# Performance work log

Measured on AMD Instinct MI355X. Metric: run time of the kernel, lower is better.

Reference implementation:

```python
import jax, jax.numpy as jnp
import numpy as np

# Static module config (matches init_kwargs; note forward requires P == Np)
Np = 60   # particles
P  = 60   # per-particle features
Nv = 14   # secondary vertices
S  = 5    # per-vertex features
De = 20
Do = 24
HID = 60
NPP = Np * (Np - 1)
NPV = Np * Nv

# Edge list replacing the dense one-hot Rr/Rs matmuls.
# Edges are all ordered pairs (i, j), i != j, ordered by receiver i then sender j,
# so edges with the same receiver are contiguous (enables reshape+sum scatter).
_pairs = np.array([(i, j) for i in range(Np) for j in range(Np) if i != j], dtype=np.int64)
RECV = jnp.asarray(_pairs[:, 0])  # [NPP]
SEND = jnp.asarray(_pairs[:, 1])  # [NPP]


def _mlp(h, W1, b1, W2, b2):
    return jax.nn.relu(h @ W1 + b1) @ W2 + b2


def setup_inputs() -> dict:
    key = jax.random.key(0)
    ks = jax.random.split(key, 9)
    B = 1024

    def lin(k, fi, fo):
        kw, kb = jax.random.split(k)
        s = 1.0 / np.sqrt(fi)
        W = jax.random.uniform(kw, (fi, fo), minval=-s, maxval=s, dtype=jnp.float32)
        b = jax.random.uniform(kb, (fo,), minval=-s, maxval=s, dtype=jnp.float32)
        return W, b

    W1_pp, b1_pp = lin(ks[0], 2 * P, HID)
    W2_pp, b2_pp = lin(ks[1], HID, De)
    W1_pv, b1_pv = lin(ks[2], P + S, HID)
    W2_pv, b2_pv = lin(ks[3], HID, De)
    W1_o, b1_o = lin(ks[4], P + De, HID)
    W2_o, b2_o = lin(ks[5], HID, Do)
    Wc, bc = lin(ks[6], Do, 1)
    x = jax.random.normal(ks[7], (B, P, Np), dtype=jnp.float32)
    y = jax.random.normal(ks[8], (B, S, Nv), dtype=jnp.float32)
    return dict(x=x, y=y,
                W1_pp=W1_pp, b1_pp=b1_pp, W2_pp=W2_pp, b2_pp=b2_pp,
                W1_pv=W1_pv, b1_pv=b1_pv, W2_pv=W2_pv, b2_pv=b2_pv,
                W1_o=W1_o, b1_o=b1_o, W2_o=W2_o, b2_o=b2_o,
                Wc=Wc, bc=bc)


def reference(x, y, W1_pp, b1_pp, W2_pp, b2_pp, W1_pv, b1_pv, W2_pv, b2_pv,
              W1_o, b1_o, W2_o, b2_o, Wc, bc):
    Bb = x.shape[0]
    # particle-particle branch: gather (x @ Rr, x @ Rs) as index takes
    Orr = jnp.take(x, RECV, axis=2)                  # [B, P, NPP]
    Ors = jnp.take(x, SEND, axis=2)                  # [B, P, NPP]
    Bcat = jnp.concatenate([Orr, Ors], axis=1)       # [B, 2P, NPP]
    # Faithful to the original: B.view(-1, 2P) WITHOUT transposing (row-major flatten)
    E = _mlp(Bcat.reshape(-1, 2 * P), W1_pp, b1_pp, W2_pp, b2_pp).reshape(Bb, NPP, De)
    E = jnp.swapaxes(E, 1, 2)                        # [B, De, NPP]
    # scatter-sum E @ Rr.T : edges grouped by receiver -> reshape+sum
    Ebar_pp = E.reshape(Bb, De, Np, Np - 1).sum(axis=-1)   # [B, De, Np]
    # particle-vertex branch: t = i*Nv + v
    Ork = jnp.repeat(x, Nv, axis=2)                  # [B, P, NPV]  (x @ Rk)
    Orv = jnp.tile(y, (1, 1, Np))                    # [B, S, NPV]  (y @ Rv)
    C = jnp.swapaxes(jnp.concatenate([Ork, Orv], axis=1), 1, 2)  # [B, NPV, P+S]
    F = _mlp(C.reshape(-1, P + S), W1_pv, b1_pv, W2_pv, b2_pv).reshape(Bb, NPV, De)
    F = jnp.swapaxes(F, 1, 2)                        # [B, De, NPV]
    Ebar_pv = F.reshape(Bb, De, Np, Nv).sum(axis=-1)  # F @ Rk.T  -> [B, De, Np]
    Ebar = jnp.swapaxes(Ebar_pp + Ebar_pv, 1, 2)     # [B, Np, De]
    J = jnp.concatenate([x, Ebar], axis=2)           # [B, Np, P+De] (requires P==Np)
    O = _mlp(J.reshape(-1, P + De), W1_o, b1_o, W2_o, b2_o).reshape(Bb, Np, Do)
    O = O.sum(axis=1)                                # transpose+sum over particles -> [B, Do]
    O = O @ Wc + bc                                  # [B, 1]
    return jax.nn.sigmoid(O)
```

## Files before the change

kernel.cpp:

```cpp
#include <hip/hip_runtime.h>
#include <hip/hip_bf16.h>
#include <math.h>

typedef __attribute__((ext_vector_type(8))) short short8;
typedef __attribute__((ext_vector_type(4))) float f32x4;

namespace {
constexpr int XP = 61;
constexpr int EB0 = 3660;
constexpr int Y0 = 4860;
constexpr int ZSLOT = 4930;
constexpr int ARENA_W = 4931;

constexpr int NTAB_PP = 222 * 4 * 64 * 8;
constexpr int NTAB_PV = 53 * 3 * 64 * 8;
constexpr int NTAB_O  = 4 * 3 * 64 * 8;
constexpr int TABPP_B = 0;
constexpr int TABPV_B = 909312;
constexpr int TABO_B  = 1072128;
constexpr int WPP1_B  = 1084416;
constexpr int WPP2_B  = 1100800;
constexpr int WPV1_B  = 1104896;
constexpr int WPV2_B  = 1117184;
constexpr int WO1_B   = 1121280;
constexpr int WO2_B   = 1133568;
constexpr int BIAS_B  = 1137664;
}

__device__ __forceinline__ short f2bfs(float f) {
  __hip_bfloat16 h = __float2bfloat16(f);
  short s;
  __builtin_memcpy(&s, &h, 2);
  return s;
}

__global__ __launch_bounds__(256) void build_tables(char* wsb) {
  int t = blockIdx.x * 256 + threadIdx.x;
  unsigned short* tpp = (unsigned short*)(wsb + TABPP_B);
  unsigned short* tpv = (unsigned short*)(wsb + TABPV_B);
  unsigned short* tou = (unsigned short*)(wsb + TABO_B);
  if (t < NTAB_PP) {
    int j = t & 7, l = (t >> 3) & 63, blk = t >> 9;
    int ks = blk & 3, mt = blk >> 2;
    int rr = mt * 16 + (l & 15), k = ks * 32 + (l >> 4) * 8 + j;
    unsigned off = ZSLOT;
    if (rr < 3540 && k < 120) {
      unsigned p = (unsigned)rr * 120u + (unsigned)k;
      unsigned f = p / 3540u, e = p - f * 3540u;
      unsigned i = e / 59u, jj = e - i * 59u;
      unsigned col = (f < 60u) ? i : ((jj < i) ? jj : jj + 1u);
      unsigned ft = (f < 60u) ? f : f - 60u;
      off = ft * (unsigned)XP + col;
    }
    tpp[t] = (unsigned short)off;
    return;
  }
  t -= NTAB_PP;
  if (t < NTAB_PV) {
    int j = t & 7, l = (t >> 3) & 63, blk = t >> 9;
    int ks = blk % 3, mt = blk / 3;
    int tt = mt * 16 + (l & 15), k = ks * 32 + (l >> 4) * 8 + j;
    unsigned off = ZSLOT;
    if (tt < 840 && k < 65) {
      int i = tt / 14, v = tt - i * 14;
      off = (k < 60) ? (unsigned)(k * XP + i) : (unsigned)(Y0 + (k - 60) * 14 + v);
    }
    tpv[t] = (unsigned short)off;
    return;
  }
  t -= NTAB_PV;
  if (t < NTAB_O) {
    int j = t & 7, l = (t >> 3) & 63, blk = t >> 9;
    int ks = blk % 3, mt = blk / 3;
    int r = mt * 16 + (l & 15), k = ks * 32 + (l >> 4) * 8 + j;
    unsigned off = ZSLOT;
    if (r < 60 && k < 80)
      off = (k < 60) ? (unsigned)(r * XP + k) : (unsigned)(EB0 + r * 20 + (k - 60));
    tou[t] = (unsigned short)off;
  }
}

__global__ __launch_bounds__(256) void build_wfrag(char* wsb,
    const float* W1pp, const float* W2pp, const float* W1pv, const float* W2pv,
    const float* W1o, const float* W2o,
    const float* b1pp, const float* b2pp, const float* b1pv, const float* b2pv,
    const float* b1o, const float* b2o) {
  int t = blockIdx.x * 256 + threadIdx.x;
  if (t < 13312) {
    const float* W; int Kt, Nt, NTt; unsigned* dst; int local;
    if (t < 4096)       { W = W1pp; Kt = 120; Nt = 60; NTt = 4; dst = (unsigned*)(wsb + WPP1_B); local = t; }
    else if (t < 5120)  { W = W2pp; Kt = 60;  Nt = 20; NTt = 2; dst = (unsigned*)(wsb + WPP2_B); local = t - 4096; }
    else if (t < 8192)  { W = W1pv; Kt = 65;  Nt = 60; NTt = 4; dst = (unsigned*)(wsb + WPV1_B); local = t - 5120; }
    else if (t < 9216)  { W = W2pv; Kt = 60;  Nt = 20; NTt = 2; dst = (unsigned*)(wsb + WPV2_B); local = t - 8192; }
    else if (t < 12288) { W = W1o;  Kt = 80;  Nt = 60; NTt = 4; dst = (unsigned*)(wsb + WO1_B);  local = t - 9216; }
    else                { W = W2o;  Kt = 60;  Nt = 24; NTt = 2; dst = (unsigned*)(wsb + WO2_B);  local = t - 12288; }
    int d = local & 3, l = (local >> 2) & 63, rest = local >> 8;
    int nt = rest % NTt, ks = rest / NTt;
    int k = ks * 32 + (l >> 4) * 8 + 2 * d, n = nt * 16 + (l & 15);
    float v0 = (k < Kt && n < Nt) ? W[k * Nt + n] : 0.f;
    float v1 = (k + 1 < Kt && n < Nt) ? W[(k + 1) * Nt + n] : 0.f;
    unsigned u0 = (unsigned short)f2bfs(v0);
    unsigned u1 = (unsigned short)f2bfs(v1);
    dst[local] = u0 | (u1 << 16);
    return;
  }
  t -= 13312;
  if (t < 288) {
    float* bd = (float*)(wsb + BIAS_B);
    float v = 0.f;
    if (t < 64)       { if (t < 60) v = b1pp[t]; }
    else if (t < 96)  { int n = t - 64;  if (n < 20) v = b2pp[n]; }
    else if (t < 160) { int n = t - 96;  if (n < 60) v = b1pv[n]; }
    else if (t < 192) { int n = t - 160; if (n < 20) v = b2pv[n]; }
    else if (t < 256) { int n = t - 192; if (n < 60) v = b1o[n]; }
    else              { int n = t - 256; if (n < 24) v = b2o[n]; }
    bd[t] = v;
  }
}

template <int NKS>
__device__ __forceinline__ void mlp_tile(
    int mt, int lane, const uint4* __restrict__ tab,
    const short8 (&bf1)[NKS * 4], const short8 (&bf2)[4],
    const float* __restrict__ biasf, int b1off, int b2off,
    const float* arena, short (*hrow)[72], f32x4 (&a2)[2]) {
  const int cl = lane & 15, qq = lane >> 4;
  f32x4 acc[4];
#pragma unroll
  for (int nt = 0; nt < 4; ++nt) {
    float bv = biasf[b1off + nt * 16 + cl];
    acc[nt] = (f32x4){bv, bv, bv, bv};
  }
#pragma unroll
  for (int ks = 0; ks < NKS; ++ks) {
    uint4 tw = tab[(mt * NKS + ks) * 64 + lane];
    float g0 = arena[tw.x & 0xffffu];
    float g1 = arena[tw.x >> 16];
    float g2 = arena[tw.y & 0xffffu];
    float g3 = arena[tw.y >> 16];
    float g4 = arena[tw.z & 0xffffu];
    float g5 = arena[tw.z >> 16];
    float g6 = arena[tw.w & 0xffffu];
    float g7 = arena[tw.w >> 16];
    short8 af;
    af[0] = f2bfs(g0); af[1] = f2bfs(g1); af[2] = f2bfs(g2); af[3] = f2bfs(g3);
    af[4] = f2bfs(g4); af[5] = f2bfs(g5); af[6] = f2bfs(g6); af[7] = f2bfs(g7);
#pragma unroll
    for (int nt = 0; nt < 4; ++nt)
      acc[nt] = __builtin_amdgcn_mfma_f32_16x16x32_bf16(af, bf1[ks * 4 + nt], acc[nt], 0, 0, 0);
  }
#pragma unroll
  for (int nt = 0; nt < 4; ++nt)
#pragma unroll
    for (int r = 0; r < 4; ++r)
      hrow[qq * 4 + r][nt * 16 + cl] = f2bfs(fmaxf(acc[nt][r], 0.f));
#pragma unroll
  for (int nt = 0; nt < 2; ++nt) {
    float bv = biasf[b2off + nt * 16 + cl];
    a2[nt] = (f32x4){bv, bv, bv, bv};
  }
#pragma unroll
  for (int k2 = 0; k2 < 2; ++k2) {
    short8 af2 = *(const short8*)&hrow[cl][k2 * 32 + qq * 8];
#pragma unroll
    for (int nt = 0; nt < 2; ++nt)
      a2[nt] = __builtin_amdgcn_mfma_f32_16x16x32_bf16(af2, bf2[k2 * 2 + nt], a2[nt], 0, 0, 0);
  }
}

__global__ __launch_bounds__(256, 2) void fused_kernel(
    const float* __restrict__ x, const float* __restrict__ y,
    const float* __restrict__ Wc, const float* __restrict__ Bc,
    const char* __restrict__ wsb, float* __restrict__ out) {
  __shared__ float arena[ARENA_W];
  __shared__ short hlds[4][16][72];
  __shared__ float osum[24];

  const int b = blockIdx.x;
  const int tid = threadIdx.x;
  const int w = tid >> 6;
  const int lane = tid & 63;
  const int cl = lane & 15, qq = lane >> 4, q4 = (lane >> 4) * 4;

  for (int k = tid; k < 3600; k += 256) {
    int r = k / 60, c = k - r * 60;
    arena[r * XP + c] = x[(size_t)b * 3600 + k];
  }
  if (tid < 70) arena[Y0 + tid] = y[(size_t)b * 70 + tid];
  for (int k = tid; k < 1200; k += 256) arena[EB0 + k] = 0.f;
  if (tid == 0) arena[ZSLOT] = 0.f;
  if (tid < 24) osum[tid] = 0.f;
  __syncthreads();

  const float* biasf = (const float*)(wsb + BIAS_B);

  {
    const short8* wf1 = (const short8*)(wsb + WPP1_B);
    const short8* wf2 = (const short8*)(wsb + WPP2_B);
    short8 bf1[16], bf2[4];
#pragma unroll
    for (int i = 0; i < 16; ++i) bf1[i] = wf1[i * 64 + lane];
#pragma unroll
    for (int i = 0; i < 4; ++i) bf2[i] = wf2[i * 64 + lane];
    const uint4* tab = (const uint4*)(wsb + TABPP_B);

    for (int mt = w; mt < 222; mt += 4) {
      f32x4 a2[2];
      mlp_tile<4>(mt, lane, tab, bf1, bf2, biasf, 0, 64, arena, hlds[w], a2);
      int rb = mt * 16 + q4;
      int riA = rb / 59, riB = (rb + 3) / 59;
#pragma unroll
      for (int nt = 0; nt < 2; ++nt) {
        int col = nt * 16 + cl;
        if (col < 20) {
          if (riA == riB && rb + 3 < 3540) {
            atomicAdd(&arena[EB0 + riA * 20 + col],
                      a2[nt][0] + a2[nt][1] + a2[nt][2] + a2[nt][3]);
          } else {
#pragma unroll
            for (int r = 0; r < 4; ++r) {
              int rr = rb + r;
              if (rr < 3540) atomicAdd(&arena[EB0 + (rr / 59) * 20 + col], a2[nt][r]);
            }
          }
        }
      }
    }
  }

  {
    const short8* wf1 = (const short8*)(wsb + WPV1_B);
    const short8* wf2 = (const short8*)(wsb + WPV2_B);
    short8 bf1[12], bf2[4];
#pragma unroll
    for (int i = 0; i < 12; ++i) bf1[i] = wf1[i * 64 + lane];
#pragma unroll
    for (int i = 0; i < 4; ++i) bf2[i] = wf2[i * 64 + lane];
    const uint4* tab = (const uint4*)(wsb + TABPV_B);

    for (int mt = w; mt < 53; mt += 4) {
      f32x4 a2[2];
      mlp_tile<3>(mt, lane, tab, bf1, bf2, biasf, 96, 160, arena, hlds[w], a2);
      int rb = mt * 16 + q4;
      int riA = rb / 14, riB = (rb + 3) / 14;
#pragma unroll
      for (int nt = 0; nt < 2; ++nt) {
        int col = nt * 16 + cl;
        if (col < 20) {
          if (riA == riB && rb + 3 < 840) {
            atomicAdd(&arena[EB0 + riA * 20 + col],
                      a2[nt][0] + a2[nt][1] + a2[nt][2] + a2[nt][3]);
          } else {
#pragma unroll
            for (int r = 0; r < 4; ++r) {
              int tt = rb + r;
              if (tt < 840) atomicAdd(&arena[EB0 + (tt / 14) * 20 + col], a2[nt][r]);
            }
          }
        }
      }
    }
  }

  __syncthreads();

  {
    const short8* wf1 = (const short8*)(wsb + WO1_B);
    const short8* wf2 = (const short8*)(wsb + WO2_B);
    short8 bf1[12], bf2[4];
#pragma unroll
    for (int i = 0; i < 12; ++i) bf1[i] = wf1[i * 64 + lane];
#pragma unroll
    for (int i = 0; i < 4; ++i) bf2[i] = wf2[i * 64 + lane];
    const uint4* tab = (const uint4*)(wsb + TABO_B);

    f32x4 a2[2];
    mlp_tile<3>(w, lane, tab, bf1, bf2, biasf, 192, 256, arena, hlds[w], a2);
    int rb = w * 16 + q4;
#pragma unroll
    for (int nt = 0; nt < 2; ++nt) {
      int col = nt * 16 + cl;
      if (col < 24) {
        if (rb + 3 < 60) {
          atomicAdd(&osum[col], a2[nt][0] + a2[nt][1] + a2[nt][2] + a2[nt][3]);
        } else {
#pragma unroll
          for (int r = 0; r < 4; ++r) {
            if (rb + r < 60) atomicAdd(&osum[col], a2[nt][r]);
          }
        }
      }
    }
  }

  __syncthreads();
  if (tid == 0) {
    float sd = Bc[0];
#pragma unroll
    for (int o = 0; o < 24; ++o) sd = fmaf(osum[o], Wc[o], sd);
    out[b] = 1.f / (1.f + expf(-sd));
  }
}

extern "C" void kernel_launch(void* const* d_in, const int* in_sizes, int n_in,
                              void* d_out, int out_size, void* d_ws, size_t ws_size,
                              hipStream_t stream) {
  const float* x     = (const float*)d_in[0];
  const float* y     = (const float*)d_in[1];
  const float* W1_pp = (const float*)d_in[2];
  const float* b1_pp = (const float*)d_in[3];
  const float* W2_pp = (const float*)d_in[4];
  const float* b2_pp = (const float*)d_in[5];
  const float* W1_pv = (const float*)d_in[6];
  const float* b1_pv = (const float*)d_in[7];
  const float* W2_pv = (const float*)d_in[8];
  const float* b2_pv = (const float*)d_in[9];
  const float* W1_o  = (const float*)d_in[10];
  const float* b1_o  = (const float*)d_in[11];
  const float* W2_o  = (const float*)d_in[12];
  const float* b2_o  = (const float*)d_in[13];
  const float* Wc    = (const float*)d_in[14];
  const float* bc    = (const float*)d_in[15];
  float* out = (float*)d_out;
  char* wsb = (char*)d_ws;

  const int Bb = in_sizes[0] / 3600;
  const int tab_total = NTAB_PP + NTAB_PV + NTAB_O;

  build_tables<<<(tab_total + 255) / 256, 256, 0, stream>>>(wsb);
  build_wfrag<<<(13600 + 255) / 256, 256, 0, stream>>>(wsb,
      W1_pp, W2_pp, W1_pv, W2_pv, W1_o, W2_o,
      b1_pp, b2_pp, b1_pv, b2_pv, b1_o, b2_o);
  fused_kernel<<<Bb, 256, 0, stream>>>(x, y, Wc, bc, wsb, out);
}
```

Baseline: 347.4 us.

## Process two MLP tiles per wave, stream weights from memory, raise occupancy

Weight fragments are no longer held in registers. They are now read from global memory on every k-step, which frees VGPRs and allows the launch bound to go from 2 to 4 blocks per CU. Each wave now processes two row tiles at a time, so one weight load feeds two MFMAs and the LDS gathers of the two tiles can interleave. The gather tables now store byte offsets to drop an address shift, and bias values are hoisted into registers. The cost is more global/L1 weight traffic per MFMA and double the LDS hidden buffer per wave, which could limit the occupancy gain.

```diff
diff --git a/kernel.cpp b/kernel.cpp
--- a/kernel.cpp
+++ b/kernel.cpp
@@ -16,15 +16,15 @@
 constexpr int NTAB_PV = 53 * 3 * 64 * 8;
 constexpr int NTAB_O  = 4 * 3 * 64 * 8;
 constexpr int TABPP_B = 0;
-constexpr int TABPV_B = 909312;
-constexpr int TABO_B  = 1072128;
-constexpr int WPP1_B  = 1084416;
-constexpr int WPP2_B  = 1100800;
-constexpr int WPV1_B  = 1104896;
-constexpr int WPV2_B  = 1117184;
-constexpr int WO1_B   = 1121280;
-constexpr int WO2_B   = 1133568;
-constexpr int BIAS_B  = 1137664;
+constexpr int TABPV_B = TABPP_B + NTAB_PP * 2;
+constexpr int TABO_B  = TABPV_B + NTAB_PV * 2;
+constexpr int WPP1_B  = TABO_B + NTAB_O * 2;
+constexpr int WPP2_B  = WPP1_B + 16 * 64 * 16;
+constexpr int WPV1_B  = WPP2_B + 4 * 64 * 16;
+constexpr int WPV2_B  = WPV1_B + 12 * 64 * 16;
+constexpr int WO1_B   = WPV2_B + 4 * 64 * 16;
+constexpr int WO2_B   = WO1_B + 12 * 64 * 16;
+constexpr int BIAS_B  = WO2_B + 4 * 64 * 16;
 }
 
 __device__ __forceinline__ short f2bfs(float f) {
@@ -52,7 +52,7 @@
       unsigned ft = (f < 60u) ? f : f - 60u;
       off = ft * (unsigned)XP + col;
     }
-    tpp[t] = (unsigned short)off;
+    tpp[t] = (unsigned short)(off * 4u);
     return;
   }
   t -= NTAB_PP;
@@ -65,7 +65,7 @@
       int i = tt / 14, v = tt - i * 14;
       off = (k < 60) ? (unsigned)(k * XP + i) : (unsigned)(Y0 + (k - 60) * 14 + v);
     }
-    tpv[t] = (unsigned short)off;
+    tpv[t] = (unsigned short)(off * 4u);
     return;
   }
   t -= NTAB_PV;
@@ -76,7 +76,7 @@
     unsigned off = ZSLOT;
     if (r < 60 && k < 80)
       off = (k < 60) ? (unsigned)(r * XP + k) : (unsigned)(EB0 + r * 20 + (k - 60));
-    tou[t] = (unsigned short)off;
+    tou[t] = (unsigned short)(off * 4u);
   }
 }
 
@@ -118,69 +118,121 @@
   }
 }
 
-template <int NKS>
-__device__ __forceinline__ void mlp_tile(
-    int mt, int lane, const uint4* __restrict__ tab,
-    const short8 (&bf1)[NKS * 4], const short8 (&bf2)[4],
-    const float* __restrict__ biasf, int b1off, int b2off,
-    const float* arena, short (*hrow)[72], f32x4 (&a2)[2]) {
+__device__ __forceinline__ short8 gather8(const char* xb, uint4 tw) {
+  float g0 = *(const float*)(xb + (tw.x & 0xffffu));
+  float g1 = *(const float*)(xb + (tw.x >> 16));
+  float g2 = *(const float*)(xb + (tw.y & 0xffffu));
+  float g3 = *(const float*)(xb + (tw.y >> 16));
+  float g4 = *(const float*)(xb + (tw.z & 0xffffu));
+  float g5 = *(const float*)(xb + (tw.z >> 16));
+  float g6 = *(const float*)(xb + (tw.w & 0xffffu));
+  float g7 = *(const float*)(xb + (tw.w >> 16));
+  short8 af;
+  af[0] = f2bfs(g0); af[1] = f2bfs(g1); af[2] = f2bfs(g2); af[3] = f2bfs(g3);
+  af[4] = f2bfs(g4); af[5] = f2bfs(g5); af[6] = f2bfs(g6); af[7] = f2bfs(g7);
+  return af;
+}
+
+template <int NKS, bool DUAL>
+__device__ __forceinline__ void mlp_tiles(
+    int mtA, int mtB, int lane,
+    const uint4* __restrict__ tab,
+    const short8* __restrict__ wf1, const short8* __restrict__ wf2,
+    const float (&b1v)[4], const float (&b2v)[2],
+    const float* arena, short (*bufA)[72], short (*bufB)[72],
+    f32x4 (&a2A)[2], f32x4 (&a2B)[2])
+{
   const int cl = lane & 15, qq = lane >> 4;
-  f32x4 acc[4];
+  const char* xb = (const char*)arena;
+
+  f32x4 accA[4], accB[4];
 #pragma unroll
   for (int nt = 0; nt < 4; ++nt) {
-    float bv = biasf[b1off + nt * 16 + cl];
-    acc[nt] = (f32x4){bv, bv, bv, bv};
-  }
+    float bv = b1v[nt];
+    accA[nt] = (f32x4){bv, bv, bv, bv};
+    if constexpr (DUAL) accB[nt] = (f32x4){bv, bv, bv, bv};
+  }
+
 #pragma unroll
   for (int ks = 0; ks < NKS; ++ks) {
-    uint4 tw = tab[(mt * NKS + ks) * 64 + lane];
-    float g0 = arena[tw.x & 0xffffu];
-    float g1 = arena[tw.x >> 16];
-    float g2 = arena[tw.y & 0xffffu];
-    float g3 = arena[tw.y >> 16];
-    float g4 = arena[tw.z & 0xffffu];
-    float g5 = arena[tw.z >> 16];
-    float g6 = arena[tw.w & 0xffffu];
-    float g7 = arena[tw.w >> 16];
-    short8 af;
-    af[0] = f2bfs(g0); af[1] = f2bfs(g1); af[2] = f2bfs(g2); af[3] = f2bfs(g3);
-    af[4] = f2bfs(g4); af[5] = f2bfs(g5); af[6] = f2bfs(g6); af[7] = f2bfs(g7);
-#pragma unroll
-    for (int nt = 0; nt < 4; ++nt)
-      acc[nt] = __builtin_amdgcn_mfma_f32_16x16x32_bf16(af, bf1[ks * 4 + nt], acc[nt], 0, 0, 0);
-  }
+    uint4 twA = tab[(mtA * NKS + ks) * 64 + lane];
+    uint4 twB;
+    if constexpr (DUAL) twB = tab[(mtB * NKS + ks) * 64 + lane];
+    short8 afA = gather8(xb, twA);
+    short8 afB;
+    if constexpr (DUAL) afB = gather8(xb, twB);
+#pragma unroll
+    for (int nt = 0; nt < 4; ++nt) {
+      short8 wf = wf1[(ks * 4 + nt) * 64 + lane];
+      accA[nt] = __builtin_amdgcn_mfma_f32_16x16x32_bf16(afA, wf, accA[nt], 0, 0, 0);
+      if constexpr (DUAL)
+        accB[nt] = __builtin_amdgcn_mfma_f32_16x16x32_bf16(afB, wf, accB[nt], 0, 0, 0);
+    }
+  }
+
 #pragma unroll
   for (int nt = 0; nt < 4; ++nt)
 #pragma unroll
-    for (int r = 0; r < 4; ++r)
-      hrow[qq * 4 + r][nt * 16 + cl] = f2bfs(fmaxf(acc[nt][r], 0.f));
+    for (int r = 0; r < 4; ++r) {
+      bufA[qq * 4 + r][nt * 16 + cl] = f2bfs(fmaxf(accA[nt][r], 0.f));
+      if constexpr (DUAL)
+        bufB[qq * 4 + r][nt * 16 + cl] = f2bfs(fmaxf(accB[nt][r], 0.f));
+    }
+
 #pragma unroll
   for (int nt = 0; nt < 2; ++nt) {
-    float bv = biasf[b2off + nt * 16 + cl];
-    a2[nt] = (f32x4){bv, bv, bv, bv};
+    float bv = b2v[nt];
+    a2A[nt] = (f32x4){bv, bv, bv, bv};
+    if constexpr (DUAL) a2B[nt] = (f32x4){bv, bv, bv, bv};
   }
 #pragma unroll
   for (int k2 = 0; k2 < 2; ++k2) {
-    short8 af2 = *(const short8*)&hrow[cl][k2 * 32 + qq * 8];
-#pragma unroll
-    for (int nt = 0; nt < 2; ++nt)
-      a2[nt] = __builtin_amdgcn_mfma_f32_16x16x32_bf16(af2, bf2[k2 * 2 + nt], a2[nt], 0, 0, 0);
-  }
-}
-
-__global__ __launch_bounds__(256, 2) void fused_kernel(
+    short8 hA = *(const short8*)&bufA[cl][k2 * 32 + qq * 8];
+    short8 hB;
+    if constexpr (DUAL) hB = *(const short8*)&bufB[cl][k2 * 32 + qq * 8];
+#pragma unroll
+    for (int nt = 0; nt < 2; ++nt) {
+      short8 wf = wf2[(k2 * 2 + nt) * 64 + lane];
+      a2A[nt] = __builtin_amdgcn_mfma_f32_16x16x32_bf16(hA, wf, a2A[nt], 0, 0, 0);
+      if constexpr (DUAL)
+        a2B[nt] = __builtin_amdgcn_mfma_f32_16x16x32_bf16(hB, wf, a2B[nt], 0, 0, 0);
+    }
+  }
+}
+
+template <int DIV, int LIM>
+__device__ __forceinline__ void scatter_e(const f32x4 (&a2)[2], int rb, float* eb, int cl) {
+  int riA = rb / DIV, riB = (rb + 3) / DIV;
+#pragma unroll
+  for (int nt = 0; nt < 2; ++nt) {
+    int col = nt * 16 + cl;
+    if (col < 20) {
+      if (riA == riB && rb + 3 < LIM) {
+        atomicAdd(&eb[riA * 20 + col], a2[nt][0] + a2[nt][1] + a2[nt][2] + a2[nt][3]);
+      } else {
+#pragma unroll
+        for (int r = 0; r < 4; ++r) {
+          int rr = rb + r;
+          if (rr < LIM) atomicAdd(&eb[(rr / DIV) * 20 + col], a2[nt][r]);
+        }
+      }
+    }
+  }
+}
+
+__global__ __launch_bounds__(256, 4) void fused_kernel(
     const float* __restrict__ x, const float* __restrict__ y,
     const float* __restrict__ Wc, const float* __restrict__ Bc,
     const char* __restrict__ wsb, float* __restrict__ out) {
   __shared__ float arena[ARENA_W];
-  __shared__ short hlds[4][16][72];
+  __shared__ short hlds[4][2][16][72];
   __shared__ float osum[24];
 
   const int b = blockIdx.x;
   const int tid = threadIdx.x;
   const int w = tid >> 6;
   const int lane = tid & 63;
-  const int cl = lane & 15, qq = lane >> 4, q4 = (lane >> 4) * 4;
+  const int cl = lane & 15, q4 = (lane >> 4) * 4;
 
   for (int k = tid; k < 3600; k += 256) {
     int r = k / 60, c = k - r * 60;
@@ -197,68 +249,52 @@
   {
     const short8* wf1 = (const short8*)(wsb + WPP1_B);
     const short8* wf2 = (const short8*)(wsb + WPP2_B);
-    short8 bf1[16], bf2[4];
-#pragma unroll
-    for (int i = 0; i < 16; ++i) bf1[i] = wf1[i * 64 + lane];
-#pragma unroll
-    for (int i = 0; i < 4; ++i) bf2[i] = wf2[i * 64 + lane];
     const uint4* tab = (const uint4*)(wsb + TABPP_B);
-
-    for (int mt = w; mt < 222; mt += 4) {
-      f32x4 a2[2];
-      mlp_tile<4>(mt, lane, tab, bf1, bf2, biasf, 0, 64, arena, hlds[w], a2);
-      int rb = mt * 16 + q4;
-      int riA = rb / 59, riB = (rb + 3) / 59;
-#pragma unroll
-      for (int nt = 0; nt < 2; ++nt) {
-        int col = nt * 16 + cl;
-        if (col < 20) {
-          if (riA == riB && rb + 3 < 3540) {
-            atomicAdd(&arena[EB0 + riA * 20 + col],
-                      a2[nt][0] + a2[nt][1] + a2[nt][2] + a2[nt][3]);
-          } else {
-#pragma unroll
-            for (int r = 0; r < 4; ++r) {
-              int rr = rb + r;
-              if (rr < 3540) atomicAdd(&arena[EB0 + (rr / 59) * 20 + col], a2[nt][r]);
-            }
-          }
-        }
-      }
+    float b1v[4], b2v[2];
+#pragma unroll
+    for (int nt = 0; nt < 4; ++nt) b1v[nt] = biasf[0 + nt * 16 + cl];
+#pragma unroll
+    for (int nt = 0; nt < 2; ++nt) b2v[nt] = biasf[64 + nt * 16 + cl];
+
+    int mt = w;
+    for (; mt + 4 < 222; mt += 8) {
+      f32x4 a2A[2], a2B[2];
+      mlp_tiles<4, true>(mt, mt + 4, lane, tab, wf1, wf2, b1v, b2v, arena,
+                         hlds[w][0], hlds[w][1], a2A, a2B);
+      scatter_e<59, 3540>(a2A, mt * 16 + q4, &arena[EB0], cl);
+      scatter_e<59, 3540>(a2B, (mt + 4) * 16 + q4, &arena[EB0], cl);
+    }
+    if (mt < 222) {
+      f32x4 a2A[2], a2B[2];
+      mlp_tiles<4, false>(mt, mt, lane, tab, wf1, wf2, b1v, b2v, arena,
+                          hlds[w][0], hlds[w][1], a2A, a2B);
+      scatter_e<59, 3540>(a2A, mt * 16 + q4, &arena[EB0], cl);
     }
   }
 
   {
     const short8* wf1 = (const short8*)(wsb + WPV1_B);
     const short8* wf2 = (const short8*)(wsb + WPV2_B);
-    short8 bf1[12], bf2[4];
-#pragma unroll
-    for (int i = 0; i < 12; ++i) bf1[i] = wf1[i * 64 + lane];
-#pragma unroll
-    for (int i = 0; i < 4; ++i) bf2[i] = wf2[i * 64 + lane];
     const uint4* tab = (const uint4*)(wsb + TABPV_B);
-
-    for (int mt = w; mt < 53; mt += 4) {
-      f32x4 a2[2];
-      mlp_tile<3>(mt, lane, tab, bf1, bf2, biasf, 96, 160, arena, hlds[w], a2);
-      int rb = mt * 16 + q4;
-      int riA = rb / 14, riB = (rb + 3) / 14;
-#pragma unroll
-      for (int nt = 0; nt < 2; ++nt) {
-        int col = nt * 16 + cl;
-        if (col < 20) {
-          if (riA == riB && rb + 3 < 840) {
-            atomicAdd(&arena[EB0 + riA * 20 + col],
-                      a2[nt][0] + a2[nt][1] + a2[nt][2] + a2[nt][3]);
-          } else {
-#pragma unroll
-            for (int r = 0; r < 4; ++r) {
-              int tt = rb + r;
-              if (tt < 840) atomicAdd(&arena[EB0 + (tt / 14) * 20 + col], a2[nt][r]);
-            }
-          }
-        }
-      }
+    float b1v[4], b2v[2];
+#pragma unroll
+    for (int nt = 0; nt < 4; ++nt) b1v[nt] = biasf[96 + nt * 16 + cl];
+#pragma unroll
+    for (int nt = 0; nt < 2; ++nt) b2v[nt] = biasf[160 + nt * 16 + cl];
+
+    int mt = w;
+    for (; mt + 4 < 53; mt += 8) {
+      f32x4 a2A[2], a2B[2];
+      mlp_tiles<3, true>(mt, mt + 4, lane, tab, wf1, wf2, b1v, b2v, arena,
+                         hlds[w][0], hlds[w][1], a2A, a2B);
+      scatter_e<14, 840>(a2A, mt * 16 + q4, &arena[EB0], cl);
+      scatter_e<14, 840>(a2B, (mt + 4) * 16 + q4, &arena[EB0], cl);
+    }
+    if (mt < 53) {
+      f32x4 a2A[2], a2B[2];
+      mlp_tiles<3, false>(mt, mt, lane, tab, wf1, wf2, b1v, b2v, arena,
+                          hlds[w][0], hlds[w][1], a2A, a2B);
+      scatter_e<14, 840>(a2A, mt * 16 + q4, &arena[EB0], cl);
     }
   }
 
@@ -267,27 +303,27 @@
   {
     const short8* wf1 = (const short8*)(wsb + WO1_B);
     const short8* wf2 = (const short8*)(wsb + WO2_B);
-    short8 bf1[12], bf2[4];
-#pragma unroll
-    for (int i = 0; i < 12; ++i) bf1[i] = wf1[i * 64 + lane];
-#pragma unroll
-    for (int i = 0; i < 4; ++i) bf2[i] = wf2[i * 64 + lane];
     const uint4* tab = (const uint4*)(wsb + TABO_B);
-
-    f32x4 a2[2];
-    mlp_tile<3>(w, lane, tab, bf1, bf2, biasf, 192, 256, arena, hlds[w], a2);
+    float b1v[4], b2v[2];
+#pragma unroll
+    for (int nt = 0; nt < 4; ++nt) b1v[nt] = biasf[192 + nt * 16 + cl];
+#pragma unroll
+    for (int nt = 0; nt < 2; ++nt) b2v[nt] = biasf[256 + nt * 16 + cl];
+
+    f32x4 a2A[2], a2B[2];
+    mlp_tiles<3, false>(w, w, lane, tab, wf1, wf2, b1v, b2v, arena,
+                        hlds[w][0], hlds[w][1], a2A, a2B);
     int rb = w * 16 + q4;
 #pragma unroll
     for (int nt = 0; nt < 2; ++nt) {
       int col = nt * 16 + cl;
       if (col < 24) {
         if (rb + 3 < 60) {
-          atomicAdd(&osum[col], a2[nt][0] + a2[nt][1] + a2[nt][2] + a2[nt][3]);
+          atomicAdd(&osum[col], a2A[nt][0] + a2A[nt][1] + a2A[nt][2] + a2A[nt][3]);
         } else {
 #pragma unroll
-          for (int r = 0; r < 4; ++r) {
-            if (rb + r < 60) atomicAdd(&osum[col], a2[nt][r]);
-          }
+          for (int r = 0; r < 4; ++r)
+            if (rb + r < 60) atomicAdd(&osum[col], a2A[nt][r]);
         }
       }
     }
```

New measurement: 534.6 us. 1.54x slower.
